# Performance work log

Measured on AMD Instinct MI355X. Metric: run time of the kernel, lower is better.

## Reference

```python
import jax, jax.numpy as jnp
import numpy as np

B, T, D, R = 4, 2048, 1024, 64  # batch, seq_len, hidden_dim, max_relative_position


def setup_inputs() -> dict:
    key = jax.random.key(0)
    ks = jax.random.split(key, 11)
    s = 1.0 / np.sqrt(D)

    def lin(k):
        return (jax.random.normal(k, (D, D), jnp.float32) * s)

    return {
        "repre": jax.random.normal(ks[0], (B, T, D), jnp.float32),
        "mask": jnp.ones((B, T, T), jnp.int32),  # 1 = valid position
        "st_Wq": lin(ks[1]), "st_bq": jnp.zeros((D,), jnp.float32),
        "st_Wk": lin(ks[2]), "st_bk": jnp.zeros((D,), jnp.float32),
        "st_rel": jax.random.normal(ks[3], (2 * R + 1, D), jnp.float32) * 0.02,
        "ed_Wq": lin(ks[4]), "ed_bq": jnp.zeros((D,), jnp.float32),
        "ed_Wk": lin(ks[5]), "ed_bk": jnp.zeros((D,), jnp.float32),
        "ed_rel": jax.random.normal(ks[6], (2 * R + 1, D), jnp.float32) * 0.02,
    }


def _attn_logits(x, Wq, bq, Wk, bk, rel, mask):
    # Single-head attention scores with relative-position key bias (OpenNMT style).
    d = x.shape[-1]
    q = (x @ Wq + bq) * (1.0 / jnp.sqrt(jnp.float32(d)))  # [B,T,D], pre-scaled query
    k = x @ Wk + bk                                        # [B,T,D]
    scores = jnp.einsum('btd,bsd->bts', q, k)              # [B,T,T] content scores
    Tn = x.shape[1]
    Rn = (rel.shape[0] - 1) // 2
    pos = jnp.arange(Tn)
    # relative position matrix: clip(j - i, -R, R) + R  -> [T,T] indices
    idx = jnp.clip(pos[None, :] - pos[:, None], -Rn, Rn) + Rn
    # q . rel_emb for every relative offset, then gather per (i,j):
    # equivalent to einsum('btd,tsd->bts', q, rel[idx]) without the [T,T,D] gather.
    qr = jnp.einsum('btd,rd->btr', q, rel)                 # [B,T,2R+1]
    scores = scores + qr[:, pos[:, None], idx]             # [B,T,T]
    return jnp.where(mask.astype(bool), scores, jnp.float32(-1e18))


def reference(repre, mask, st_Wq, st_bq, st_Wk, st_bk, st_rel,
              ed_Wq, ed_bq, ed_Wk, ed_bk, ed_rel):
    span_st_logits = _attn_logits(repre, st_Wq, st_bq, st_Wk, st_bk, st_rel, mask)
    span_ed_logits = _attn_logits(repre, ed_Wq, ed_bq, ed_Wk, ed_bk, ed_rel, mask)
    return (span_st_logits, span_ed_logits)
```

## Files before the change

### kernel.cpp

```cpp
#include <hip/hip_runtime.h>

constexpr int Bn = 4;
constexpr int Tn = 2048;
constexpr int Dn = 1024;
constexpr int Rn = 64;
constexpr int RELP = 256;
constexpr int QR_STRIDE = 132;

typedef __bf16 bf8 __attribute__((ext_vector_type(8)));
typedef float f32x4 __attribute__((ext_vector_type(4)));

__device__ __forceinline__ unsigned short f2bf(float f) {
    unsigned int u = __float_as_uint(f);
    u += 0x7fffu + ((u >> 16) & 1u);
    return (unsigned short)(u >> 16);
}

#define GLDS(g, l)                                                            \
    __builtin_amdgcn_global_load_lds(                                         \
        (const __attribute__((address_space(1))) void*)(g),                   \
        (__attribute__((address_space(3))) void*)(l), 16, 0, 0)

__device__ __forceinline__ void mfma_gemm_128(
    const unsigned short* __restrict__ Ab,
    const unsigned short* __restrict__ Bb,
    int K, f32x4 acc[4][4],
    unsigned short* As, unsigned short* Bs)
{
    const int tid = threadIdx.x;
    const int r0  = tid >> 2;
    const int c8  = (tid & 3) * 8;
    const int lane = tid & 63;
    const int w    = tid >> 6;
    const int wm = (w & 1) * 64, wn = (w >> 1) * 64;
    const int l15 = lane & 15, lq = lane >> 4;

    for (int k0 = 0; k0 < K; k0 += 32) {
        __syncthreads();
        GLDS(Ab + (size_t)r0 * K + k0 + c8,        As + r0 * 32 + c8);
        GLDS(Ab + ((size_t)r0 + 64) * K + k0 + c8, As + (r0 + 64) * 32 + c8);
        GLDS(Bb + (size_t)r0 * K + k0 + c8,        Bs + r0 * 32 + c8);
        GLDS(Bb + ((size_t)r0 + 64) * K + k0 + c8, Bs + (r0 + 64) * 32 + c8);
        __syncthreads();
        bf8 a[4], b[4];
#pragma unroll
        for (int i = 0; i < 4; ++i) {
            a[i] = *(const bf8*)&As[(wm + i * 16 + l15) * 32 + lq * 8];
            b[i] = *(const bf8*)&Bs[(wn + i * 16 + l15) * 32 + lq * 8];
        }
#pragma unroll
        for (int i = 0; i < 4; ++i)
#pragma unroll
            for (int j = 0; j < 4; ++j)
                acc[i][j] = __builtin_amdgcn_mfma_f32_16x16x32_bf16(
                    a[i], b[j], acc[i][j], 0, 0, 0);
    }
}

__global__ __launch_bounds__(256) void cvt_bf16(
    const float* __restrict__ in, unsigned short* __restrict__ out, int n4)
{
    int i = blockIdx.x * 256 + threadIdx.x;
    if (i < n4) {
        float4 v = ((const float4*)in)[i];
        ushort4 o;
        o.x = f2bf(v.x); o.y = f2bf(v.y); o.z = f2bf(v.z); o.w = f2bf(v.w);
        ((ushort4*)out)[i] = o;
    }
}

__global__ __launch_bounds__(256) void wt_transpose(
    const float* __restrict__ w0, const float* __restrict__ w1,
    const float* __restrict__ w2, const float* __restrict__ w3,
    unsigned short* __restrict__ WT)
{
    __shared__ float t[32][33];
    const int z = blockIdx.z;
    const float* W = z == 0 ? w0 : z == 1 ? w1 : z == 2 ? w2 : w3;
    const int x = blockIdx.x * 32 + threadIdx.x;
    const int y0 = blockIdx.y * 32;
#pragma unroll
    for (int j = 0; j < 32; j += 8)
        t[threadIdx.y + j][threadIdx.x] = W[(size_t)(y0 + threadIdx.y + j) * Dn + x];
    __syncthreads();
    unsigned short* o = WT + (size_t)z * Dn * Dn;
    const int n0 = blockIdx.x * 32;
#pragma unroll
    for (int j = 0; j < 32; j += 8)
        o[(size_t)(n0 + threadIdx.y + j) * Dn + y0 + threadIdx.x] =
            f2bf(t[threadIdx.x][threadIdx.y + j]);
}

__global__ __launch_bounds__(256) void rel_pad(
    const float* __restrict__ st_rel, const float* __restrict__ ed_rel,
    unsigned short* __restrict__ relb)
{
    const int z = blockIdx.y;
    const float* in = z ? ed_rel : st_rel;
    const int i4 = blockIdx.x * 256 + threadIdx.x;
    const int row = (i4 * 4) >> 10;
    const int col = (i4 * 4) & 1023;
    ushort4 o; o.x = 0; o.y = 0; o.z = 0; o.w = 0;
    if (row < 2 * Rn + 1) {
        float4 v = *(const float4*)(in + (size_t)row * 1024 + col);
        o.x = f2bf(v.x); o.y = f2bf(v.y); o.z = f2bf(v.z); o.w = f2bf(v.w);
    }
    ((ushort4*)(relb + (size_t)z * RELP * 1024))[i4] = o;
}

__global__ __launch_bounds__(256) void proj_gemm(
    const unsigned short* __restrict__ Xb, const unsigned short* __restrict__ Wb,
    const float* __restrict__ b0, const float* __restrict__ b1,
    const float* __restrict__ b2, const float* __restrict__ b3,
    unsigned short* __restrict__ outQK, float qscale)
{
    __shared__ unsigned short As[128 * 32], Bs[128 * 32];
    const int z = blockIdx.z;
    const float* bias = z == 0 ? b0 : z == 1 ? b1 : z == 2 ? b2 : b3;
    const float scale = (z & 1) ? 1.0f : qscale;

    const unsigned short* Ab = Xb + (size_t)blockIdx.x * 128 * Dn;
    const unsigned short* Bb = Wb + ((size_t)z * Dn + blockIdx.y * 128) * Dn;

    f32x4 zero = {0.f, 0.f, 0.f, 0.f};
    f32x4 acc[4][4];
#pragma unroll
    for (int i = 0; i < 4; ++i)
#pragma unroll
        for (int j = 0; j < 4; ++j) acc[i][j] = zero;

    mfma_gemm_128(Ab, Bb, Dn, acc, As, Bs);

    const int tid = threadIdx.x, lane = tid & 63, w = tid >> 6;
    const int wm = (w & 1) * 64, wn = (w >> 1) * 64;
    const int l15 = lane & 15, lq = lane >> 4;
    unsigned short* out = outQK + (size_t)z * (size_t)Bn * Tn * Dn;

#pragma unroll
    for (int ni = 0; ni < 4; ++ni) {
        const int col = blockIdx.y * 128 + wn + ni * 16 + l15;
        const float bv = bias[col];
#pragma unroll
        for (int mi = 0; mi < 4; ++mi) {
#pragma unroll
            for (int r = 0; r < 4; ++r) {
                const int row = blockIdx.x * 128 + wm + mi * 16 + lq * 4 + r;
                out[(size_t)row * Dn + col] = f2bf((acc[mi][ni][r] + bv) * scale);
            }
        }
    }
}

__global__ __launch_bounds__(256) void qr_gemm(
    const unsigned short* __restrict__ QKb, const unsigned short* __restrict__ relb,
    float* __restrict__ QR)
{
    __shared__ unsigned short As[128 * 32], Bs[128 * 32];
    const int z = blockIdx.z;
    const unsigned short* Ab = QKb + ((size_t)(z * 2) * Bn * Tn + blockIdx.x * 128) * Dn;
    const unsigned short* Bb = relb + ((size_t)z * RELP + blockIdx.y * 128) * Dn;

    f32x4 zero = {0.f, 0.f, 0.f, 0.f};
    f32x4 acc[4][4];
#pragma unroll
    for (int i = 0; i < 4; ++i)
#pragma unroll
        for (int j = 0; j < 4; ++j) acc[i][j] = zero;

    mfma_gemm_128(Ab, Bb, Dn, acc, As, Bs);

    const int tid = threadIdx.x, lane = tid & 63, w = tid >> 6;
    const int wm = (w & 1) * 64, wn = (w >> 1) * 64;
    const int l15 = lane & 15, lq = lane >> 4;
    float* out = QR + (size_t)z * (size_t)Bn * Tn * QR_STRIDE;

#pragma unroll
    for (int ni = 0; ni < 4; ++ni) {
        const int col = blockIdx.y * 128 + wn + ni * 16 + l15;
        if (col >= 2 * Rn + 1) continue;
#pragma unroll
        for (int mi = 0; mi < 4; ++mi) {
#pragma unroll
            for (int r = 0; r < 4; ++r) {
                const int row = blockIdx.x * 128 + wm + mi * 16 + lq * 4 + r;
                out[(size_t)row * QR_STRIDE + col] = acc[mi][ni][r];
            }
        }
    }
}

__global__ __launch_bounds__(256) void scores_gemm(
    const unsigned short* __restrict__ QKb, const float* __restrict__ QR,
    const int* __restrict__ mask, float* __restrict__ Out)
{
    __shared__ unsigned short As[128 * 32], Bs[128 * 32];
    const int z = blockIdx.z;
    const int side = z >> 2, bt = z & 3;

    const unsigned short* Ab =
        QKb + ((size_t)side * 2 * Bn * Tn + (size_t)bt * Tn + blockIdx.x * 128) * Dn;
    const unsigned short* Bb =
        QKb + (((size_t)side * 2 + 1) * Bn * Tn + (size_t)bt * Tn + blockIdx.y * 128) * Dn;
    const float* QRb = QR + ((size_t)side * Bn * Tn + (size_t)bt * Tn) * QR_STRIDE;
    const int* maskb = mask + (size_t)bt * Tn * Tn;
    float* outb = Out + ((size_t)side * Bn + bt) * (size_t)Tn * Tn;

    f32x4 zero = {0.f, 0.f, 0.f, 0.f};
    f32x4 acc[4][4];
#pragma unroll
    for (int i = 0; i < 4; ++i)
#pragma unroll
        for (int j = 0; j < 4; ++j) acc[i][j] = zero;

    mfma_gemm_128(Ab, Bb, Dn, acc, As, Bs);

    const int tid = threadIdx.x, lane = tid & 63, w = tid >> 6;
    const int wm = (w & 1) * 64, wn = (w >> 1) * 64;
    const int l15 = lane & 15, lq = lane >> 4;

#pragma unroll
    for (int mi = 0; mi < 4; ++mi) {
#pragma unroll
        for (int r = 0; r < 4; ++r) {
            const int i = blockIdx.x * 128 + wm + mi * 16 + lq * 4 + r;
            const float* qrow = QRb + (size_t)i * QR_STRIDE;
            const int* mrow = maskb + (size_t)i * Tn;
            float* orow = outb + (size_t)i * Tn;
#pragma unroll
            for (int ni = 0; ni < 4; ++ni) {
                const int j = blockIdx.y * 128 + wn + ni * 16 + l15;
                int d = j - i;
                d = d < -Rn ? -Rn : (d > Rn ? Rn : d);
                const float qv = qrow[d + Rn];
                orow[j] = mrow[j] ? acc[mi][ni][r] + qv : -1e18f;
            }
        }
    }
}

extern "C" void kernel_launch(void* const* d_in, const int* in_sizes, int n_in,
                              void* d_out, int out_size, void* d_ws, size_t ws_size,
                              hipStream_t stream) {
    const float* repre  = (const float*)d_in[0];
    const int*   mask   = (const int*)  d_in[1];
    const float* st_Wq  = (const float*)d_in[2];
    const float* st_bq  = (const float*)d_in[3];
    const float* st_Wk  = (const float*)d_in[4];
    const float* st_bk  = (const float*)d_in[5];
    const float* st_rel = (const float*)d_in[6];
    const float* ed_Wq  = (const float*)d_in[7];
    const float* ed_bq  = (const float*)d_in[8];
    const float* ed_Wk  = (const float*)d_in[9];
    const float* ed_bk  = (const float*)d_in[10];
    const float* ed_rel = (const float*)d_in[11];
    float* out = (float*)d_out;

    const size_t MT = (size_t)Bn * Tn;

    unsigned short* Xb   = (unsigned short*)d_ws;
    unsigned short* Wb   = Xb + MT * Dn;
    unsigned short* relb = Wb + (size_t)4 * Dn * Dn;
    unsigned short* QKb  = relb + (size_t)2 * RELP * Dn;
    float* QRbuf = (float*)(QKb + (size_t)4 * MT * Dn);

    const float qscale = 0.03125f;
    dim3 blk(256);

    {
        int n4 = (int)(MT * Dn / 4);
        cvt_bf16<<<dim3((n4 + 255) / 256), blk, 0, stream>>>(repre, Xb, n4);
        wt_transpose<<<dim3(32, 32, 4), dim3(32, 8), 0, stream>>>(
            st_Wq, st_Wk, ed_Wq, ed_Wk, Wb);
        rel_pad<<<dim3(RELP * Dn / 4 / 256, 2), blk, 0, stream>>>(st_rel, ed_rel, relb);
    }

    proj_gemm<<<dim3((int)MT / 128, Dn / 128, 4), blk, 0, stream>>>(
        Xb, Wb, st_bq, st_bk, ed_bq, ed_bk, QKb, qscale);

    qr_gemm<<<dim3((int)MT / 128, RELP / 128, 2), blk, 0, stream>>>(QKb, relb, QRbuf);

    scores_gemm<<<dim3(Tn / 128, Tn / 128, 8), blk, 0, stream>>>(QKb, QRbuf, mask, out);
}
```

Baseline: 532.1 us.

## Double-buffer LDS tiles in shared MFMA GEMM loop to overlap loads

The shared 128x128 MFMA GEMM helper now keeps two LDS buffers per operand. It issues the global-to-LDS async loads for the next K-tile before computing on the current one, so each iteration needs one barrier instead of two. The goal is to hide global load latency behind the MFMA work in the projection, relative-position and score GEMMs. This doubles LDS use per block to 32 KB, which may reduce occupancy.

After: 557.8 us. +4.8%, slower.

```diff
diff --git a/kernel.cpp b/kernel.cpp
--- a/kernel.cpp
+++ b/kernel.cpp
@@ -35,18 +35,30 @@
     const int wm = (w & 1) * 64, wn = (w >> 1) * 64;
     const int l15 = lane & 15, lq = lane >> 4;
 
-    for (int k0 = 0; k0 < K; k0 += 32) {
-        __syncthreads();
-        GLDS(Ab + (size_t)r0 * K + k0 + c8,        As + r0 * 32 + c8);
-        GLDS(Ab + ((size_t)r0 + 64) * K + k0 + c8, As + (r0 + 64) * 32 + c8);
-        GLDS(Bb + (size_t)r0 * K + k0 + c8,        Bs + r0 * 32 + c8);
-        GLDS(Bb + ((size_t)r0 + 64) * K + k0 + c8, Bs + (r0 + 64) * 32 + c8);
-        __syncthreads();
+    const int nt = K >> 5;
+
+    GLDS(Ab + (size_t)r0 * K + c8,        As + r0 * 32 + c8);
+    GLDS(Ab + ((size_t)r0 + 64) * K + c8, As + (r0 + 64) * 32 + c8);
+    GLDS(Bb + (size_t)r0 * K + c8,        Bs + r0 * 32 + c8);
+    GLDS(Bb + ((size_t)r0 + 64) * K + c8, Bs + (r0 + 64) * 32 + c8);
+    __syncthreads();
+
+    int cur = 0;
+    for (int t = 0; t < nt; ++t) {
+        if (t + 1 < nt) {
+            const int k0 = (t + 1) << 5;
+            const int nb = (cur ^ 1) * (128 * 32);
+            GLDS(Ab + (size_t)r0 * K + k0 + c8,        As + nb + r0 * 32 + c8);
+            GLDS(Ab + ((size_t)r0 + 64) * K + k0 + c8, As + nb + (r0 + 64) * 32 + c8);
+            GLDS(Bb + (size_t)r0 * K + k0 + c8,        Bs + nb + r0 * 32 + c8);
+            GLDS(Bb + ((size_t)r0 + 64) * K + k0 + c8, Bs + nb + (r0 + 64) * 32 + c8);
+        }
+        const int cb = cur * (128 * 32);
         bf8 a[4], b[4];
 #pragma unroll
         for (int i = 0; i < 4; ++i) {
-            a[i] = *(const bf8*)&As[(wm + i * 16 + l15) * 32 + lq * 8];
-            b[i] = *(const bf8*)&Bs[(wn + i * 16 + l15) * 32 + lq * 8];
+            a[i] = *(const bf8*)&As[cb + (wm + i * 16 + l15) * 32 + lq * 8];
+            b[i] = *(const bf8*)&Bs[cb + (wn + i * 16 + l15) * 32 + lq * 8];
         }
 #pragma unroll
         for (int i = 0; i < 4; ++i)
@@ -54,6 +66,8 @@
             for (int j = 0; j < 4; ++j)
                 acc[i][j] = __builtin_amdgcn_mfma_f32_16x16x32_bf16(
                     a[i], b[j], acc[i][j], 0, 0, 0);
+        __syncthreads();
+        cur ^= 1;
     }
 }
 
@@ -114,7 +128,7 @@
     const float* __restrict__ b2, const float* __restrict__ b3,
     unsigned short* __restrict__ outQK, float qscale)
 {
-    __shared__ unsigned short As[128 * 32], Bs[128 * 32];
+    __shared__ unsigned short As[2 * 128 * 32], Bs[2 * 128 * 32];
     const int z = blockIdx.z;
     const float* bias = z == 0 ? b0 : z == 1 ? b1 : z == 2 ? b2 : b3;
     const float scale = (z & 1) ? 1.0f : qscale;
@@ -155,7 +169,7 @@
     const unsigned short* __restrict__ QKb, const unsigned short* __restrict__ relb,
     float* __restrict__ QR)
 {
-    __shared__ unsigned short As[128 * 32], Bs[128 * 32];
+    __shared__ unsigned short As[2 * 128 * 32], Bs[2 * 128 * 32];
     const int z = blockIdx.z;
     const unsigned short* Ab = QKb + ((size_t)(z * 2) * Bn * Tn + blockIdx.x * 128) * Dn;
     const unsigned short* Bb = relb + ((size_t)z * RELP + blockIdx.y * 128) * Dn;
@@ -193,7 +207,7 @@
     const unsigned short* __restrict__ QKb, const float* __restrict__ QR,
     const int* __restrict__ mask, float* __restrict__ Out)
 {
-    __shared__ unsigned short As[128 * 32], Bs[128 * 32];
+    __shared__ unsigned short As[2 * 128 * 32], Bs[2 * 128 * 32];
     const int z = blockIdx.z;
     const int side = z >> 2, bt = z & 3;
 
```
